# Kernel tuning notes

Measured on AMD Instinct MI355X. Metric: run time of the kernel, lower is better.

Reference implementation:

```python
import jax, jax.numpy as jnp
import numpy as np

# Llama-7B FFN up-proj quantized with HQQ 4-bit, group_size=64, axis=0
OUT, IN, GS = 11008, 4096, 64
G = OUT * IN // GS  # 704512 groups


def setup_inputs() -> dict:
    key = jax.random.key(0)
    k1, k2, k3, k4, k5 = jax.random.split(key, 5)
    # packed 4-bit weights: two nibbles per byte, shape [GS//2, G]
    W_q = jax.random.randint(k1, (GS // 2, G), 0, 256, dtype=jnp.int32)
    # per-group scale (meta['scale'] = 1/scale from quantize) and zero
    scale = jax.random.uniform(k2, (1, G), jnp.float32, minval=1e-3, maxval=1e-2)
    zero = jax.random.uniform(k3, (1, G), jnp.float32, minval=0.0, maxval=15.0)
    # decode-style activations: 8 sequences, 1 token each
    x = jax.random.normal(k4, (8, 1, IN), dtype=jnp.float32)
    bias = jax.random.normal(k5, (OUT,), dtype=jnp.float32) * 0.01
    return {"W_q": W_q, "scale": scale, "zero": zero, "x": x, "bias": bias}


def reference(W_q, scale, zero, x, bias):
    # BitPack.unpack_4bit_u8: high nibble rows stacked on low nibble rows
    hi = (W_q >> 4) & 0xF
    lo = W_q & 0xF
    W_q_p = jnp.concatenate([hi, lo], axis=0).astype(x.dtype)  # [GS, G]
    # Quantizer.dequantize: (W_q_p - zero) * scale, reshape to weight shape
    W_r = ((W_q_p - zero) * scale).reshape(OUT, IN)  # [out, in]
    # torch.nn.functional.linear(x, W_r, bias)
    return jnp.einsum('bsi,oi->bso', x, W_r) + bias
```

## Files before the change

kernel.cpp:

```cpp
#include <hip/hip_runtime.h>


#define OUT_ 11008
#define IN_ 4096
#define G_ 704512
#define OC_ 172

__global__ __launch_bounds__(256, 4)
void hqq_gemv(const int* __restrict__ Wq, const float* __restrict__ scale,
              const float* __restrict__ zero, const float* __restrict__ x,
              const float* __restrict__ bias, float* __restrict__ out) {
    const int lane = threadIdx.x;
    const int ty   = threadIdx.y;
    const int oc   = blockIdx.y;
    const int rq0  = blockIdx.x * 8 + ty * 2;

    float acc[4][8];
#pragma unroll
    for (int r = 0; r < 4; ++r)
#pragma unroll
        for (int b = 0; b < 8; ++b) acc[r][b] = 0.f;

    const long gbase = (long)oc * IN_;
    const int* __restrict__ wqA = Wq + (long)rq0 * G_ + gbase;
    const int* __restrict__ wqB = Wq + (long)(rq0 + 1) * G_ + gbase;
    const float* __restrict__ sp = scale + gbase;
    const float* __restrict__ zp = zero + gbase;

    for (int k0 = 0; k0 < IN_; k0 += 256) {
        const int i = k0 + lane * 4;
        const float4 s4 = *(const float4*)(sp + i);
        const float4 z4 = *(const float4*)(zp + i);
        float4 xv[8];
#pragma unroll
        for (int b = 0; b < 8; ++b)
            xv[b] = *(const float4*)(x + b * IN_ + i);

#pragma unroll
        for (int rr = 0; rr < 2; ++rr) {
            const int4 q4 = *(const int4*)((rr ? wqB : wqA) + i);
            const int   qs[4] = {q4.x, q4.y, q4.z, q4.w};
            const float ss[4] = {s4.x, s4.y, s4.z, s4.w};
            const float zz[4] = {z4.x, z4.y, z4.z, z4.w};
            float wh[4], wl[4];
#pragma unroll
            for (int j = 0; j < 4; ++j) {
                wh[j] = ((float)((qs[j] >> 4) & 0xF) - zz[j]) * ss[j];
                wl[j] = ((float)(qs[j] & 0xF) - zz[j]) * ss[j];
            }
#pragma unroll
            for (int b = 0; b < 8; ++b) {
                const float4 xb = xv[b];
                float ah = acc[rr * 2 + 0][b];
                float al = acc[rr * 2 + 1][b];
                ah = fmaf(xb.x, wh[0], ah);
                ah = fmaf(xb.y, wh[1], ah);
                ah = fmaf(xb.z, wh[2], ah);
                ah = fmaf(xb.w, wh[3], ah);
                al = fmaf(xb.x, wl[0], al);
                al = fmaf(xb.y, wl[1], al);
                al = fmaf(xb.z, wl[2], al);
                al = fmaf(xb.w, wl[3], al);
                acc[rr * 2 + 0][b] = ah;
                acc[rr * 2 + 1][b] = al;
            }
        }
    }

#pragma unroll
    for (int r = 0; r < 4; ++r)
#pragma unroll
        for (int b = 0; b < 8; ++b) {
            float v = acc[r][b];
#pragma unroll
            for (int off = 32; off > 0; off >>= 1)
                v += __shfl_down(v, off, 64);
            acc[r][b] = v;
        }

    if (lane == 0) {
#pragma unroll
        for (int rr = 0; rr < 2; ++rr) {
            const int rq = rq0 + rr;
            const int o_hi = rq * OC_ + oc;
            const int o_lo = (rq + 32) * OC_ + oc;
            const float bh = bias[o_hi];
            const float bl = bias[o_lo];
#pragma unroll
            for (int b = 0; b < 8; ++b) {
                out[b * OUT_ + o_hi] = acc[rr * 2 + 0][b] + bh;
                out[b * OUT_ + o_lo] = acc[rr * 2 + 1][b] + bl;
            }
        }
    }
}

extern "C" void kernel_launch(void* const* d_in, const int* in_sizes, int n_in,
                              void* d_out, int out_size, void* d_ws, size_t ws_size,
                              hipStream_t stream) {
    const int*   Wq    = (const int*)d_in[0];
    const float* scale = (const float*)d_in[1];
    const float* zero  = (const float*)d_in[2];
    const float* x     = (const float*)d_in[3];
    const float* bias  = (const float*)d_in[4];
    float* out = (float*)d_out;

    dim3 grid(4, OC_);
    dim3 block(64, 4);
    hqq_gemv<<<grid, block, 0, stream>>>(Wq, scale, zero, x, bias, out);
}
```

Before: 155.8 us.

## Split K across two blocks with atomic accumulation and prefetch weights

Splits the K dimension into two halves across a third grid dimension, doubling the block count. Partial sums are combined with atomicAdd into an output that a separate kernel zeroes first, and the bias is added only by the first split. The loop is fully unrolled with software prefetch of the next packed weights, and dequantization is folded into a single fma using a precomputed -zero*scale. The trade-offs are an extra kernel launch, atomic traffic, and nondeterministic summation order.

```diff
diff --git a/kernel.cpp b/kernel.cpp
--- a/kernel.cpp
+++ b/kernel.cpp
@@ -6,6 +6,11 @@
 #define G_ 704512
 #define OC_ 172
 
+__global__ void zero_out_kernel(float* __restrict__ out) {
+    const int t = blockIdx.x * 256 + threadIdx.x;
+    if (t < 8 * OUT_) out[t] = 0.f;
+}
+
 __global__ __launch_bounds__(256, 4)
 void hqq_gemv(const int* __restrict__ Wq, const float* __restrict__ scale,
               const float* __restrict__ zero, const float* __restrict__ x,
@@ -13,7 +18,16 @@
     const int lane = threadIdx.x;
     const int ty   = threadIdx.y;
     const int oc   = blockIdx.y;
+    const int ks   = blockIdx.z;
     const int rq0  = blockIdx.x * 8 + ty * 2;
+
+    const int kbase = ks * (IN_ / 2);
+    const long gb = (long)oc * IN_ + kbase;
+    const int* __restrict__ wqA = Wq + (long)rq0 * G_ + gb;
+    const int* __restrict__ wqB = wqA + G_;
+    const float* __restrict__ sp = scale + gb;
+    const float* __restrict__ zp = zero + gb;
+    const float* __restrict__ xp = x + kbase;
 
     float acc[4][8];
 #pragma unroll
@@ -21,50 +35,47 @@
 #pragma unroll
         for (int b = 0; b < 8; ++b) acc[r][b] = 0.f;
 
-    const long gbase = (long)oc * IN_;
-    const int* __restrict__ wqA = Wq + (long)rq0 * G_ + gbase;
-    const int* __restrict__ wqB = Wq + (long)(rq0 + 1) * G_ + gbase;
-    const float* __restrict__ sp = scale + gbase;
-    const float* __restrict__ zp = zero + gbase;
+    int i = lane * 4;
+    int4 qa = *(const int4*)(wqA + i);
+    int4 qb = *(const int4*)(wqB + i);
 
-    for (int k0 = 0; k0 < IN_; k0 += 256) {
-        const int i = k0 + lane * 4;
+#pragma unroll
+    for (int it = 0; it < 8; ++it) {
         const float4 s4 = *(const float4*)(sp + i);
         const float4 z4 = *(const float4*)(zp + i);
-        float4 xv[8];
+        int4 qa_n, qb_n;
+        if (it < 7) {
+            qa_n = *(const int4*)(wqA + i + 256);
+            qb_n = *(const int4*)(wqB + i + 256);
+        }
+        const float ss[4] = {s4.x, s4.y, s4.z, s4.w};
+        const float zs[4] = {-z4.x * s4.x, -z4.y * s4.y, -z4.z * s4.z, -z4.w * s4.w};
+        const int qsA[4] = {qa.x, qa.y, qa.z, qa.w};
+        const int qsB[4] = {qb.x, qb.y, qb.z, qb.w};
+
+        float w[4][4];
 #pragma unroll
-        for (int b = 0; b < 8; ++b)
-            xv[b] = *(const float4*)(x + b * IN_ + i);
-
+        for (int j = 0; j < 4; ++j) {
+            w[0][j] = fmaf((float)((qsA[j] >> 4) & 0xF), ss[j], zs[j]);
+            w[1][j] = fmaf((float)( qsA[j]       & 0xF), ss[j], zs[j]);
+            w[2][j] = fmaf((float)((qsB[j] >> 4) & 0xF), ss[j], zs[j]);
+            w[3][j] = fmaf((float)( qsB[j]       & 0xF), ss[j], zs[j]);
+        }
 #pragma unroll
-        for (int rr = 0; rr < 2; ++rr) {
-            const int4 q4 = *(const int4*)((rr ? wqB : wqA) + i);
-            const int   qs[4] = {q4.x, q4.y, q4.z, q4.w};
-            const float ss[4] = {s4.x, s4.y, s4.z, s4.w};
-            const float zz[4] = {z4.x, z4.y, z4.z, z4.w};
-            float wh[4], wl[4];
+        for (int b = 0; b < 8; ++b) {
+            const float4 xb = *(const float4*)(xp + b * IN_ + i);
 #pragma unroll
-            for (int j = 0; j < 4; ++j) {
-                wh[j] = ((float)((qs[j] >> 4) & 0xF) - zz[j]) * ss[j];
-                wl[j] = ((float)(qs[j] & 0xF) - zz[j]) * ss[j];
-            }
-#pragma unroll
-            for (int b = 0; b < 8; ++b) {
-                const float4 xb = xv[b];
-                float ah = acc[rr * 2 + 0][b];
-                float al = acc[rr * 2 + 1][b];
-                ah = fmaf(xb.x, wh[0], ah);
-                ah = fmaf(xb.y, wh[1], ah);
-                ah = fmaf(xb.z, wh[2], ah);
-                ah = fmaf(xb.w, wh[3], ah);
-                al = fmaf(xb.x, wl[0], al);
-                al = fmaf(xb.y, wl[1], al);
-                al = fmaf(xb.z, wl[2], al);
-                al = fmaf(xb.w, wl[3], al);
-                acc[rr * 2 + 0][b] = ah;
-                acc[rr * 2 + 1][b] = al;
+            for (int r = 0; r < 4; ++r) {
+                float a = acc[r][b];
+                a = fmaf(xb.x, w[r][0], a);
+                a = fmaf(xb.y, w[r][1], a);
+                a = fmaf(xb.z, w[r][2], a);
+                a = fmaf(xb.w, w[r][3], a);
+                acc[r][b] = a;
             }
         }
+        if (it < 7) { qa = qa_n; qb = qb_n; }
+        i += 256;
     }
 
 #pragma unroll
@@ -79,18 +90,14 @@
         }
 
     if (lane == 0) {
+        const int o[4] = {rq0 * OC_ + oc, (rq0 + 32) * OC_ + oc,
+                          (rq0 + 1) * OC_ + oc, (rq0 + 33) * OC_ + oc};
 #pragma unroll
-        for (int rr = 0; rr < 2; ++rr) {
-            const int rq = rq0 + rr;
-            const int o_hi = rq * OC_ + oc;
-            const int o_lo = (rq + 32) * OC_ + oc;
-            const float bh = bias[o_hi];
-            const float bl = bias[o_lo];
+        for (int r = 0; r < 4; ++r) {
+            const float bb = (ks == 0) ? bias[o[r]] : 0.f;
 #pragma unroll
-            for (int b = 0; b < 8; ++b) {
-                out[b * OUT_ + o_hi] = acc[rr * 2 + 0][b] + bh;
-                out[b * OUT_ + o_lo] = acc[rr * 2 + 1][b] + bl;
-            }
+            for (int b = 0; b < 8; ++b)
+                atomicAdd(out + b * OUT_ + o[r], acc[r][b] + bb);
         }
     }
 }
@@ -105,7 +112,9 @@
     const float* bias  = (const float*)d_in[4];
     float* out = (float*)d_out;
 
-    dim3 grid(4, OC_);
+    zero_out_kernel<<<(8 * OUT_ + 255) / 256, 256, 0, stream>>>(out);
+
+    dim3 grid(4, OC_, 2);
     dim3 block(64, 4);
     hqq_gemv<<<grid, block, 0, stream>>>(Wq, scale, zero, x, bias, out);
 }
```

After: 177.4 us. 13.8% more time.
